# Performance work log

Measured on AMD Instinct MI355X. Metric: run time of the kernel, lower is better.

Reference implementation:

```python
import jax, jax.numpy as jnp
import numpy as np

B, S, D, H, N = 1024, 2, 1, 128, 128  # batch, static_size, dynamic_size, hidden, num_nodes


def setup_inputs() -> dict:
    key = jax.random.key(0)
    ks = jax.random.split(key, 16)

    def xav(k, shape):
        fan = shape[0] + shape[1]
        lim = jnp.sqrt(6.0 / fan)
        return jax.random.uniform(k, shape, jnp.float32, -lim, lim)

    return {
        "static": jax.random.uniform(ks[0], (B, S, N), jnp.float32),
        "dynamic": jax.random.uniform(ks[1], (B, D, N), jnp.float32),
        # encoders (Conv1d kernel_size=1 == pointwise linear)
        "enc_s_w": xav(ks[2], (H, S)), "enc_s_b": jnp.zeros((H,), jnp.float32),
        "enc_d_w": xav(ks[3], (H, D)), "enc_d_b": jnp.zeros((H,), jnp.float32),
        # decoder params
        "x0": xav(ks[4], (1, S)),
        "emb_w": xav(ks[5], (H, S)), "emb_b": jnp.zeros((H,), jnp.float32),
        "w_ih": xav(ks[6], (3 * H, H)), "w_hh": xav(ks[7], (3 * H, H)),
        "b_ih": jnp.zeros((3 * H,), jnp.float32), "b_hh": jnp.zeros((3 * H,), jnp.float32),
        "attn_v": xav(ks[8], (1, H)), "attn_W": xav(ks[9], (H, 3 * H)),
        "dec_v": xav(ks[10], (1, H)), "dec_W": xav(ks[11], (H, 2 * H)),
    }


def _gru_cell(x, h, w_ih, w_hh, b_ih, b_hh):
    gi = x @ w_ih.T + b_ih  # [B, 3H]
    gh = h @ w_hh.T + b_hh
    i_r, i_z, i_n = jnp.split(gi, 3, axis=-1)
    h_r, h_z, h_n = jnp.split(gh, 3, axis=-1)
    r = jax.nn.sigmoid(i_r + h_r)
    z = jax.nn.sigmoid(i_z + h_z)
    n = jnp.tanh(i_n + r * h_n)
    return (1.0 - z) * n + z * h


def reference(static, dynamic, enc_s_w, enc_s_b, enc_d_w, enc_d_b, x0,
              emb_w, emb_b, w_ih, w_hh, b_ih, b_hh, attn_v, attn_W, dec_v, dec_W):
    # encoders: pointwise conv
    static_enc = jnp.einsum('hs,bsn->bhn', enc_s_w, static) + enc_s_b[None, :, None]
    dynamic_enc = jnp.einsum('hd,bdn->bhn', enc_d_w, dynamic) + enc_d_b[None, :, None]

    h0 = jnp.zeros((static.shape[0], H), jnp.float32)
    out0 = jnp.broadcast_to(x0, (static.shape[0], S))

    def step(carry, _):
        h, last_out = carry
        emb = last_out @ emb_w.T + emb_b                     # [B,H]
        h = _gru_cell(emb, h, w_ih, w_hh, b_ih, b_hh)        # [B,H]
        hid = jnp.broadcast_to(h[:, :, None], static_enc.shape)
        energy = jnp.concatenate([static_enc, dynamic_enc, hid], axis=1)   # [B,3H,N]
        u = jnp.tanh(jnp.einsum('hk,bkn->bhn', attn_W, energy))
        attn = jax.nn.softmax(jnp.einsum('h,bhn->bn', attn_v[0], u), axis=1)
        context = jnp.einsum('bn,bhn->bh', attn, static_enc)
        ctx = jnp.broadcast_to(context[:, :, None], static_enc.shape)
        energy2 = jnp.concatenate([static_enc, ctx], axis=1)               # [B,2H,N]
        u2 = jnp.tanh(jnp.einsum('hk,bkn->bhn', dec_W, energy2))
        logits = jnp.einsum('h,bhn->bn', dec_v[0], u2)
        probs = jax.nn.softmax(logits, axis=1)  # mask is all-ones -> log(mask)=0
        ptr = jnp.argmax(probs, axis=1)                       # [B]
        logp = jnp.log(jnp.max(probs, axis=1))
        last_out = jnp.take_along_axis(static, ptr[:, None, None], axis=2)[:, :, 0]
        return (h, last_out), (ptr, logp)

    (_, _), (ptrs, logps) = jax.lax.scan(step, (h0, out0), None, length=N)
    tour_idx = ptrs.T            # [B, N]
    tour_logp = logps.T.sum(axis=1)  # [B]
    return tour_idx, tour_logp
```

## Files before the change

kernel.cpp:

```cpp
#include <hip/hip_runtime.h>


#define H128 128
#define N128 128
#define B1024 1024
#define SC 2.885390081777927f

__device__ __forceinline__ float sigmoid_acc(float x){
    return 1.f / (1.f + expf(-x));
}
__device__ __forceinline__ float tanh_ps(float xs){
    float e = exp2f(xs);
    float r = __builtin_amdgcn_rcpf(e + 1.f);
    return fmaf(-2.f, r, 1.f);
}

__global__ void prep_kernel(const float* __restrict__ enc_s_w, const float* __restrict__ enc_s_b,
                            const float* __restrict__ enc_d_w, const float* __restrict__ enc_d_b,
                            const float* __restrict__ emb_w,   const float* __restrict__ emb_b,
                            const float* __restrict__ w_ih,    const float* __restrict__ b_ih,
                            const float* __restrict__ b_hh,
                            const float* __restrict__ attn_v,  const float* __restrict__ attn_W,
                            const float* __restrict__ dec_v,   const float* __restrict__ dec_W,
                            float4* __restrict__ A4, float4* __restrict__ D4,
                            float4* __restrict__ Q4, float4* __restrict__ G4)
{
    const int tid = threadIdx.x;
    const int blk = blockIdx.x;
    if (blk < 3){
        const int j = blk*128 + tid;
        const float* w = w_ih + j*H128;
        float a = 0.f, b = 0.f, c = 0.f;
        for (int k = 0; k < H128; ++k){
            float wv = w[k];
            a = fmaf(wv, emb_w[2*k],   a);
            b = fmaf(wv, emb_w[2*k+1], b);
            c = fmaf(wv, emb_b[k],     c);
        }
        G4[j] = make_float4(a, b, c + b_ih[j], b_hh[j]);
    } else {
        const int h = tid;
        const float* aw = attn_W + h*384;
        float u0=0.f, u1=0.f, u2=0.f, c1=0.f;
        for (int k = 0; k < H128; ++k){
            float w = aw[k];
            u0 = fmaf(w, enc_s_w[2*k],   u0);
            u1 = fmaf(w, enc_s_w[2*k+1], u1);
            c1 = fmaf(w, enc_s_b[k],     c1);
        }
        for (int k = 0; k < H128; ++k){
            float w = aw[128+k];
            u2 = fmaf(w, enc_d_w[k], u2);
            c1 = fmaf(w, enc_d_b[k], c1);
        }
        A4[h] = make_float4(SC*u0, SC*u1, SC*u2, attn_v[h]);
        const float* dw = dec_W + h*256;
        float v0=0.f, v1=0.f, c2=0.f, q0=0.f, q1=0.f;
        for (int k = 0; k < H128; ++k){
            float w = dw[k];
            v0 = fmaf(w, enc_s_w[2*k],   v0);
            v1 = fmaf(w, enc_s_w[2*k+1], v1);
            c2 = fmaf(w, enc_s_b[k],     c2);
        }
        for (int k = 0; k < H128; ++k){
            float w = dw[128+k];
            q0 = fmaf(w, enc_s_w[2*k],   q0);
            q1 = fmaf(w, enc_s_w[2*k+1], q1);
            c2 = fmaf(w, enc_s_b[k],     c2);
        }
        D4[h] = make_float4(SC*v0, SC*v1, dec_v[h], 0.f);
        Q4[h] = make_float4(SC*q0, SC*q1, SC*c2, SC*c1);
    }
}

__global__ void tp_kernel(const float* __restrict__ whh, const float* __restrict__ attnW,
                          float* __restrict__ WT, float* __restrict__ AT)
{
    const int idx = blockIdx.x*256 + threadIdx.x;
    if (idx < 49152){
        const int k = idx / 384, r = idx - k*384;
        WT[idx] = whh[r*H128 + k];
    } else {
        const int i2 = idx - 49152;
        const int k = i2 >> 7, j = i2 & 127;
        AT[i2] = SC * attnW[j*384 + 256 + k];
    }
}

__global__ __launch_bounds__(256, 2)
void decode_kernel(const float* __restrict__ statc, const float* __restrict__ dyn,
                   const float* __restrict__ x0,
                   const float* __restrict__ WT, const float* __restrict__ AT,
                   const float4* __restrict__ A4g, const float4* __restrict__ D4g,
                   const float4* __restrict__ Q4g, const float4* __restrict__ G4g,
                   float* __restrict__ out)
{
    __shared__ __align__(16) float hbuf[2][2][H128];
    __shared__ float gpre[2][5][H128];
    __shared__ __align__(16) float ahl[2][H128], chl[2][H128];
    __shared__ float s0l[2][N128], s1l[2][N128];
    __shared__ float red[2][2][8];

    const int tid = threadIdx.x;
    const int g   = tid >> 7;
    const int jl  = tid & 127;
    const int wv  = (tid >> 6) & 1;
    const int b   = blockIdx.x*2 + g;

    const int  gate1 = tid >> 7;
    const int  j1    = tid & 127;
    const bool loA   = (tid < 128);
    const float4 Gv1 = G4g[tid];
    const float4 Gv2 = G4g[256 + j1];

    const float4 qv = Q4g[jl];
    const float q0r = qv.x, q1r = qv.y, c2r = qv.z, c1r = qv.w;

    const float s0n = statc[b*256 + jl];
    const float s1n = statc[b*256 + 128 + jl];
    const float d0n = dyn[b*128 + jl];
    s0l[g][jl] = s0n; s1l[g][jl] = s1n;
    hbuf[0][g][jl] = 0.f;
    float hreg = 0.f;
    float l00 = x0[0], l01 = x0[1];
    float l10 = l00,   l11 = l01;

    float logp = 0.f;
    int cur = 0;
    __syncthreads();

    for (int t = 0; t < N128; ++t){
        const float4* h0v = (const float4*)&hbuf[cur][0][0];
        const float4* h1v = (const float4*)&hbuf[cur][1][0];
        {
            const float* pW = WT + tid;
            float a0 = 0.f, a1 = 0.f;
            #pragma unroll 4
            for (int k4 = 0; k4 < 32; ++k4){
                float4 h0 = h0v[k4], h1 = h1v[k4];
                float w0 = pW[(4*k4+0)*384];
                float w1 = pW[(4*k4+1)*384];
                float w2 = pW[(4*k4+2)*384];
                float w3 = pW[(4*k4+3)*384];
                a0 = fmaf(w0,h0.x, fmaf(w1,h0.y, fmaf(w2,h0.z, fmaf(w3,h0.w, a0))));
                a1 = fmaf(w0,h1.x, fmaf(w1,h1.y, fmaf(w2,h1.z, fmaf(w3,h1.w, a1))));
            }
            float gi0 = fmaf(Gv1.x, l00, fmaf(Gv1.y, l01, Gv1.z));
            float gi1 = fmaf(Gv1.x, l10, fmaf(Gv1.y, l11, Gv1.z));
            gpre[0][gate1][j1] = gi0 + (a0 + Gv1.w);
            gpre[1][gate1][j1] = gi1 + (a1 + Gv1.w);
        }
        {
            const float* pW = WT + 256 + j1;
            const int koff = gate1 * 16;
            float a0 = 0.f, a1 = 0.f;
            #pragma unroll 4
            for (int ki = 0; ki < 16; ++ki){
                const int k4 = koff + ki;
                float4 h0 = h0v[k4], h1 = h1v[k4];
                float w0 = pW[(4*k4+0)*384];
                float w1 = pW[(4*k4+1)*384];
                float w2 = pW[(4*k4+2)*384];
                float w3 = pW[(4*k4+3)*384];
                a0 = fmaf(w0,h0.x, fmaf(w1,h0.y, fmaf(w2,h0.z, fmaf(w3,h0.w, a0))));
                a1 = fmaf(w0,h1.x, fmaf(w1,h1.y, fmaf(w2,h1.z, fmaf(w3,h1.w, a1))));
            }
            if (loA){
                gpre[0][2][j1] = a0 + Gv2.w;
                gpre[1][2][j1] = a1 + Gv2.w;
                gpre[0][3][j1] = fmaf(Gv2.x, l00, fmaf(Gv2.y, l01, Gv2.z));
                gpre[1][3][j1] = fmaf(Gv2.x, l10, fmaf(Gv2.y, l11, Gv2.z));
            } else {
                gpre[0][4][j1] = a0;
                gpre[1][4][j1] = a1;
            }
        }
        __syncthreads();
        {
            float r  = sigmoid_acc(gpre[g][0][jl]);
            float z  = sigmoid_acc(gpre[g][1][jl]);
            float accn = gpre[g][2][jl] + gpre[g][4][jl];
            float nn = tanhf(gpre[g][3][jl] + r * accn);
            float hnew = (1.f - z) * nn + z * hreg;
            hbuf[cur^1][g][jl] = hnew; hreg = hnew;
        }
        __syncthreads();
        cur ^= 1;
        {
            const float4* hn4 = (const float4*)&hbuf[cur][g][0];
            const float* pA = AT + jl;
            float acc = c1r;
            #pragma unroll 4
            for (int k4 = 0; k4 < 32; ++k4){
                float4 hv = hn4[k4];
                acc = fmaf(pA[(4*k4+0)*128], hv.x, acc);
                acc = fmaf(pA[(4*k4+1)*128], hv.y, acc);
                acc = fmaf(pA[(4*k4+2)*128], hv.z, acc);
                acc = fmaf(pA[(4*k4+3)*128], hv.w, acc);
            }
            ahl[g][jl] = acc;
        }
        __syncthreads();
        const float4* ah4 = (const float4*)&ahl[g][0];
        float sc = 0.f;
        #pragma unroll 2
        for (int k = 0; k < 32; ++k){
            float4 ah = ah4[k];
            { float4 a = A4g[4*k+0]; float tt = fmaf(a.x,s0n, fmaf(a.y,s1n, fmaf(a.z,d0n, ah.x))); sc = fmaf(tanh_ps(tt), a.w, sc); }
            { float4 a = A4g[4*k+1]; float tt = fmaf(a.x,s0n, fmaf(a.y,s1n, fmaf(a.z,d0n, ah.y))); sc = fmaf(tanh_ps(tt), a.w, sc); }
            { float4 a = A4g[4*k+2]; float tt = fmaf(a.x,s0n, fmaf(a.y,s1n, fmaf(a.z,d0n, ah.z))); sc = fmaf(tanh_ps(tt), a.w, sc); }
            { float4 a = A4g[4*k+3]; float tt = fmaf(a.x,s0n, fmaf(a.y,s1n, fmaf(a.z,d0n, ah.w))); sc = fmaf(tanh_ps(tt), a.w, sc); }
        }
        float e  = __expf(sc);
        float se = e, sa = e * s0n, sb = e * s1n;
        #pragma unroll
        for (int off = 32; off > 0; off >>= 1){
            se += __shfl_xor(se, off, 64);
            sa += __shfl_xor(sa, off, 64);
            sb += __shfl_xor(sb, off, 64);
        }
        if ((tid & 63) == 0){ red[g][wv][0]=se; red[g][wv][1]=sa; red[g][wv][2]=sb; }
        __syncthreads();
        {
            float ssum = red[g][0][0] + red[g][1][0];
            float sat  = red[g][0][1] + red[g][1][1];
            float sbt  = red[g][0][2] + red[g][1][2];
            float cs0 = sat / ssum;
            float cs1 = sbt / ssum;
            chl[g][jl] = fmaf(q0r, cs0, fmaf(q1r, cs1, c2r));
        }
        __syncthreads();
        const float4* ch4 = (const float4*)&chl[g][0];
        float lg = 0.f;
        #pragma unroll 2
        for (int k = 0; k < 32; ++k){
            float4 ch = ch4[k];
            { float4 dd = D4g[4*k+0]; float tt = fmaf(dd.x,s0n, fmaf(dd.y,s1n, ch.x)); lg = fmaf(tanh_ps(tt), dd.z, lg); }
            { float4 dd = D4g[4*k+1]; float tt = fmaf(dd.x,s0n, fmaf(dd.y,s1n, ch.y)); lg = fmaf(tanh_ps(tt), dd.z, lg); }
            { float4 dd = D4g[4*k+2]; float tt = fmaf(dd.x,s0n, fmaf(dd.y,s1n, ch.z)); lg = fmaf(tanh_ps(tt), dd.z, lg); }
            { float4 dd = D4g[4*k+3]; float tt = fmaf(dd.x,s0n, fmaf(dd.y,s1n, ch.w)); lg = fmaf(tanh_ps(tt), dd.z, lg); }
        }
        float v = lg; int bi = jl;
        #pragma unroll
        for (int off = 32; off > 0; off >>= 1){
            float ov = __shfl_xor(v, off, 64);
            int   oi = __shfl_xor(bi, off, 64);
            if (ov > v || (ov == v && oi < bi)){ v = ov; bi = oi; }
        }
        float e2 = __expf(lg - v);
        #pragma unroll
        for (int off = 32; off > 0; off >>= 1) e2 += __shfl_xor(e2, off, 64);
        if ((tid & 63) == 0){ red[g][wv][4]=v; red[g][wv][5]=__int_as_float(bi); red[g][wv][6]=e2; }
        __syncthreads();
        int ptrs[2];
        #pragma unroll
        for (int gg = 0; gg < 2; ++gg){
            float va = red[gg][0][4], vb = red[gg][1][4];
            int   ia = __float_as_int(red[gg][0][5]), ib = __float_as_int(red[gg][1][5]);
            ptrs[gg] = (va > vb || (va == vb && ia < ib)) ? ia : ib;
        }
        {
            float va = red[g][0][4], vb = red[g][1][4];
            int   ia = __float_as_int(red[g][0][5]), ib = __float_as_int(red[g][1][5]);
            float s2a = red[g][0][6], s2b = red[g][1][6];
            float m2; int ptr;
            if (va > vb || (va == vb && ia < ib)){ m2 = va; ptr = ia; } else { m2 = vb; ptr = ib; }
            float sum2 = fmaf(s2a, __expf(va - m2), s2b * __expf(vb - m2));
            logp -= logf(sum2);
            if (jl == 0) out[b*N128 + t] = (float)ptr;
        }
        l00 = s0l[0][ptrs[0]]; l01 = s1l[0][ptrs[0]];
        l10 = s0l[1][ptrs[1]]; l11 = s1l[1][ptrs[1]];
    }
    if (jl == 0) out[B1024*N128 + b] = logp;
}

extern "C" void kernel_launch(void* const* d_in, const int* in_sizes, int n_in,
                              void* d_out, int out_size, void* d_ws, size_t ws_size,
                              hipStream_t stream)
{
    const float* statc   = (const float*)d_in[0];
    const float* dyn     = (const float*)d_in[1];
    const float* enc_s_w = (const float*)d_in[2];
    const float* enc_s_b = (const float*)d_in[3];
    const float* enc_d_w = (const float*)d_in[4];
    const float* enc_d_b = (const float*)d_in[5];
    const float* x0      = (const float*)d_in[6];
    const float* emb_w   = (const float*)d_in[7];
    const float* emb_b   = (const float*)d_in[8];
    const float* w_ih    = (const float*)d_in[9];
    const float* w_hh    = (const float*)d_in[10];
    const float* b_ih    = (const float*)d_in[11];
    const float* b_hh    = (const float*)d_in[12];
    const float* attn_v  = (const float*)d_in[13];
    const float* attn_W  = (const float*)d_in[14];
    const float* dec_v   = (const float*)d_in[15];
    const float* dec_W   = (const float*)d_in[16];

    float* ws = (float*)d_ws;
    float4* A4 = (float4*)(ws);
    float4* D4 = (float4*)(ws + 512);
    float4* Q4 = (float4*)(ws + 1024);
    float4* G4 = (float4*)(ws + 1536);
    float*  WT = ws + 3072;
    float*  AT = ws + 3072 + 49152;

    prep_kernel<<<dim3(4), dim3(128), 0, stream>>>(
        enc_s_w, enc_s_b, enc_d_w, enc_d_b, emb_w, emb_b,
        w_ih, b_ih, b_hh, attn_v, attn_W, dec_v, dec_W,
        A4, D4, Q4, G4);

    tp_kernel<<<dim3(256), dim3(256), 0, stream>>>(w_hh, attn_W, WT, AT);

    decode_kernel<<<dim3(B1024/2), dim3(256), 0, stream>>>(
        statc, dyn, x0, WT, AT,
        A4, D4, Q4, G4, (float*)d_out);
}
```

Baseline: 2.755 ms.

## Double threads per block by splitting reductions over k across thread halves

The decode kernel now runs 512 threads per block instead of 256. Each GRU matvec, attention projection and the two tanh-score loops have their k-range split across two or four thread groups, with partial sums written to shared memory and combined by the first 256 threads. The aim is to shorten the serial per-step critical path of the 128-step recurrence by adding parallelism. In exchange it adds extra __syncthreads barriers and shared-memory partial-sum traffic, leaves half the threads idle during the elementwise and reduction phases, and tightens the register budget through the new launch bounds.

```diff
diff --git a/kernel.cpp b/kernel.cpp
--- a/kernel.cpp
+++ b/kernel.cpp
@@ -87,7 +87,7 @@
     }
 }
 
-__global__ __launch_bounds__(256, 2)
+__global__ __launch_bounds__(512, 4)
 void decode_kernel(const float* __restrict__ statc, const float* __restrict__ dyn,
                    const float* __restrict__ x0,
                    const float* __restrict__ WT, const float* __restrict__ AT,
@@ -96,36 +96,43 @@
                    float* __restrict__ out)
 {
     __shared__ __align__(16) float hbuf[2][2][H128];
-    __shared__ float gpre[2][5][H128];
-    __shared__ __align__(16) float ahl[2][H128], chl[2][H128];
+    __shared__ float gprz[2][2][256];
+    __shared__ float gprn[2][4][H128];
+    __shared__ float ahp[2][4][H128];
+    __shared__ __align__(16) float ahl[2][H128];
+    __shared__ __align__(16) float chl[2][H128];
+    __shared__ float scp[2][2][H128];
     __shared__ float s0l[2][N128], s1l[2][N128];
     __shared__ float red[2][2][8];
 
     const int tid = threadIdx.x;
-    const int g   = tid >> 7;
-    const int jl  = tid & 127;
-    const int wv  = (tid >> 6) & 1;
-    const int b   = blockIdx.x*2 + g;
-
-    const int  gate1 = tid >> 7;
-    const int  j1    = tid & 127;
-    const bool loA   = (tid < 128);
-    const float4 Gv1 = G4g[tid];
-    const float4 Gv2 = G4g[256 + j1];
-
-    const float4 qv = Q4g[jl];
-    const float q0r = qv.x, q1r = qv.y, c2r = qv.z, c1r = qv.w;
-
-    const float s0n = statc[b*256 + jl];
-    const float s1n = statc[b*256 + 128 + jl];
-    const float d0n = dyn[b*128 + jl];
-    s0l[g][jl] = s0n; s1l[g][jl] = s1n;
-    hbuf[0][g][jl] = 0.f;
-    float hreg = 0.f;
-    float l00 = x0[0], l01 = x0[1];
-    float l10 = l00,   l11 = l01;
-
-    float logp = 0.f;
+    const int mg  = tid >> 8;
+    const int mn  = tid & 127;
+    const int hi  = (tid >> 7) & 1;
+    const int q   = (tid >> 7) & 3;
+    const int rowa  = tid & 255;
+    const int halfa = mg;
+    const int b0  = blockIdx.x*2;
+
+    const float s0n = statc[(b0+mg)*256 + mn];
+    const float s1n = statc[(b0+mg)*256 + 128 + mn];
+    const float d0n = dyn[(b0+mg)*128 + mn];
+    s0l[mg][mn] = s0n; s1l[mg][mn] = s1n;
+
+    const int cg = tid >> 7;
+    const int cn = tid & 127;
+    const int wvi = (tid >> 6) & 1;
+    float4 Gr = make_float4(0,0,0,0), Gz = Gr, Gn = Gr, qv = Gr;
+    float cs0n = 0.f, cs1n = 0.f, hreg = 0.f, lA = 0.f, lB = 0.f, logp = 0.f;
+    if (tid < 256){
+        Gr = G4g[cn]; Gz = G4g[128+cn]; Gn = G4g[256+cn];
+        qv = Q4g[cn];
+        cs0n = statc[(b0+cg)*256 + cn];
+        cs1n = statc[(b0+cg)*256 + 128 + cn];
+        hbuf[0][cg][cn] = 0.f;
+        lA = x0[0]; lB = x0[1];
+    }
+
     int cur = 0;
     __syncthreads();
 
@@ -133,10 +140,11 @@
         const float4* h0v = (const float4*)&hbuf[cur][0][0];
         const float4* h1v = (const float4*)&hbuf[cur][1][0];
         {
-            const float* pW = WT + tid;
+            const float* pW = WT + rowa;
             float a0 = 0.f, a1 = 0.f;
             #pragma unroll 4
-            for (int k4 = 0; k4 < 32; ++k4){
+            for (int ki = 0; ki < 16; ++ki){
+                const int k4 = halfa*16 + ki;
                 float4 h0 = h0v[k4], h1 = h1v[k4];
                 float w0 = pW[(4*k4+0)*384];
                 float w1 = pW[(4*k4+1)*384];
@@ -145,18 +153,15 @@
                 a0 = fmaf(w0,h0.x, fmaf(w1,h0.y, fmaf(w2,h0.z, fmaf(w3,h0.w, a0))));
                 a1 = fmaf(w0,h1.x, fmaf(w1,h1.y, fmaf(w2,h1.z, fmaf(w3,h1.w, a1))));
             }
-            float gi0 = fmaf(Gv1.x, l00, fmaf(Gv1.y, l01, Gv1.z));
-            float gi1 = fmaf(Gv1.x, l10, fmaf(Gv1.y, l11, Gv1.z));
-            gpre[0][gate1][j1] = gi0 + (a0 + Gv1.w);
-            gpre[1][gate1][j1] = gi1 + (a1 + Gv1.w);
-        }
-        {
-            const float* pW = WT + 256 + j1;
-            const int koff = gate1 * 16;
+            gprz[0][halfa][rowa] = a0;
+            gprz[1][halfa][rowa] = a1;
+        }
+        {
+            const float* pW = WT + 256 + mn;
             float a0 = 0.f, a1 = 0.f;
             #pragma unroll 4
-            for (int ki = 0; ki < 16; ++ki){
-                const int k4 = koff + ki;
+            for (int ki = 0; ki < 8; ++ki){
+                const int k4 = q*8 + ki;
                 float4 h0 = h0v[k4], h1 = h1v[k4];
                 float w0 = pW[(4*k4+0)*384];
                 float w1 = pW[(4*k4+1)*384];
@@ -165,114 +170,130 @@
                 a0 = fmaf(w0,h0.x, fmaf(w1,h0.y, fmaf(w2,h0.z, fmaf(w3,h0.w, a0))));
                 a1 = fmaf(w0,h1.x, fmaf(w1,h1.y, fmaf(w2,h1.z, fmaf(w3,h1.w, a1))));
             }
-            if (loA){
-                gpre[0][2][j1] = a0 + Gv2.w;
-                gpre[1][2][j1] = a1 + Gv2.w;
-                gpre[0][3][j1] = fmaf(Gv2.x, l00, fmaf(Gv2.y, l01, Gv2.z));
-                gpre[1][3][j1] = fmaf(Gv2.x, l10, fmaf(Gv2.y, l11, Gv2.z));
-            } else {
-                gpre[0][4][j1] = a0;
-                gpre[1][4][j1] = a1;
-            }
-        }
-        __syncthreads();
-        {
-            float r  = sigmoid_acc(gpre[g][0][jl]);
-            float z  = sigmoid_acc(gpre[g][1][jl]);
-            float accn = gpre[g][2][jl] + gpre[g][4][jl];
-            float nn = tanhf(gpre[g][3][jl] + r * accn);
+            gprn[0][q][mn] = a0;
+            gprn[1][q][mn] = a1;
+        }
+        __syncthreads();
+        if (tid < 256){
+            float accr = gprz[cg][0][cn]     + gprz[cg][1][cn];
+            float accz = gprz[cg][0][128+cn] + gprz[cg][1][128+cn];
+            float accn = (gprn[cg][0][cn]+gprn[cg][1][cn]) + (gprn[cg][2][cn]+gprn[cg][3][cn]);
+            float gir = fmaf(Gr.x, lA, fmaf(Gr.y, lB, Gr.z));
+            float giz = fmaf(Gz.x, lA, fmaf(Gz.y, lB, Gz.z));
+            float gin = fmaf(Gn.x, lA, fmaf(Gn.y, lB, Gn.z));
+            float r  = sigmoid_acc(gir + (accr + Gr.w));
+            float z  = sigmoid_acc(giz + (accz + Gz.w));
+            float nn = tanhf(gin + r * (accn + Gn.w));
             float hnew = (1.f - z) * nn + z * hreg;
-            hbuf[cur^1][g][jl] = hnew; hreg = hnew;
+            hbuf[cur^1][cg][cn] = hnew; hreg = hnew;
         }
         __syncthreads();
         cur ^= 1;
         {
-            const float4* hn4 = (const float4*)&hbuf[cur][g][0];
-            const float* pA = AT + jl;
-            float acc = c1r;
+            const float4* hn0 = (const float4*)&hbuf[cur][0][0];
+            const float4* hn1 = (const float4*)&hbuf[cur][1][0];
+            const float* pA = AT + mn;
+            float a0 = 0.f, a1 = 0.f;
             #pragma unroll 4
-            for (int k4 = 0; k4 < 32; ++k4){
-                float4 hv = hn4[k4];
-                acc = fmaf(pA[(4*k4+0)*128], hv.x, acc);
-                acc = fmaf(pA[(4*k4+1)*128], hv.y, acc);
-                acc = fmaf(pA[(4*k4+2)*128], hv.z, acc);
-                acc = fmaf(pA[(4*k4+3)*128], hv.w, acc);
-            }
-            ahl[g][jl] = acc;
-        }
-        __syncthreads();
-        const float4* ah4 = (const float4*)&ahl[g][0];
-        float sc = 0.f;
-        #pragma unroll 2
-        for (int k = 0; k < 32; ++k){
-            float4 ah = ah4[k];
-            { float4 a = A4g[4*k+0]; float tt = fmaf(a.x,s0n, fmaf(a.y,s1n, fmaf(a.z,d0n, ah.x))); sc = fmaf(tanh_ps(tt), a.w, sc); }
-            { float4 a = A4g[4*k+1]; float tt = fmaf(a.x,s0n, fmaf(a.y,s1n, fmaf(a.z,d0n, ah.y))); sc = fmaf(tanh_ps(tt), a.w, sc); }
-            { float4 a = A4g[4*k+2]; float tt = fmaf(a.x,s0n, fmaf(a.y,s1n, fmaf(a.z,d0n, ah.z))); sc = fmaf(tanh_ps(tt), a.w, sc); }
-            { float4 a = A4g[4*k+3]; float tt = fmaf(a.x,s0n, fmaf(a.y,s1n, fmaf(a.z,d0n, ah.w))); sc = fmaf(tanh_ps(tt), a.w, sc); }
-        }
-        float e  = __expf(sc);
-        float se = e, sa = e * s0n, sb = e * s1n;
-        #pragma unroll
-        for (int off = 32; off > 0; off >>= 1){
-            se += __shfl_xor(se, off, 64);
-            sa += __shfl_xor(sa, off, 64);
-            sb += __shfl_xor(sb, off, 64);
-        }
-        if ((tid & 63) == 0){ red[g][wv][0]=se; red[g][wv][1]=sa; red[g][wv][2]=sb; }
-        __syncthreads();
-        {
-            float ssum = red[g][0][0] + red[g][1][0];
-            float sat  = red[g][0][1] + red[g][1][1];
-            float sbt  = red[g][0][2] + red[g][1][2];
+            for (int ki = 0; ki < 8; ++ki){
+                const int k4 = q*8 + ki;
+                float4 hv0 = hn0[k4], hv1 = hn1[k4];
+                float w0 = pA[(4*k4+0)*128];
+                float w1 = pA[(4*k4+1)*128];
+                float w2 = pA[(4*k4+2)*128];
+                float w3 = pA[(4*k4+3)*128];
+                a0 = fmaf(w0,hv0.x, fmaf(w1,hv0.y, fmaf(w2,hv0.z, fmaf(w3,hv0.w, a0))));
+                a1 = fmaf(w0,hv1.x, fmaf(w1,hv1.y, fmaf(w2,hv1.z, fmaf(w3,hv1.w, a1))));
+            }
+            ahp[0][q][mn] = a0;
+            ahp[1][q][mn] = a1;
+        }
+        __syncthreads();
+        if (tid < 256){
+            ahl[cg][cn] = ((ahp[cg][0][cn]+ahp[cg][1][cn]) + (ahp[cg][2][cn]+ahp[cg][3][cn])) + qv.w;
+        }
+        __syncthreads();
+        {
+            const float4* ah4 = (const float4*)&ahl[mg][0];
+            float sc = 0.f;
+            #pragma unroll 2
+            for (int kk = 0; kk < 16; ++kk){
+                const int k = hi*16 + kk;
+                float4 ah = ah4[k];
+                { float4 a = A4g[4*k+0]; float tt = fmaf(a.x,s0n, fmaf(a.y,s1n, fmaf(a.z,d0n, ah.x))); sc = fmaf(tanh_ps(tt), a.w, sc); }
+                { float4 a = A4g[4*k+1]; float tt = fmaf(a.x,s0n, fmaf(a.y,s1n, fmaf(a.z,d0n, ah.y))); sc = fmaf(tanh_ps(tt), a.w, sc); }
+                { float4 a = A4g[4*k+2]; float tt = fmaf(a.x,s0n, fmaf(a.y,s1n, fmaf(a.z,d0n, ah.z))); sc = fmaf(tanh_ps(tt), a.w, sc); }
+                { float4 a = A4g[4*k+3]; float tt = fmaf(a.x,s0n, fmaf(a.y,s1n, fmaf(a.z,d0n, ah.w))); sc = fmaf(tanh_ps(tt), a.w, sc); }
+            }
+            scp[mg][hi][mn] = sc;
+        }
+        __syncthreads();
+        if (tid < 256){
+            float sc = scp[cg][0][cn] + scp[cg][1][cn];
+            float e  = __expf(sc);
+            float se = e, sa = e * cs0n, sb = e * cs1n;
+            #pragma unroll
+            for (int off = 32; off > 0; off >>= 1){
+                se += __shfl_xor(se, off, 64);
+                sa += __shfl_xor(sa, off, 64);
+                sb += __shfl_xor(sb, off, 64);
+            }
+            if ((tid & 63) == 0){ red[cg][wvi][0]=se; red[cg][wvi][1]=sa; red[cg][wvi][2]=sb; }
+        }
+        __syncthreads();
+        if (tid < 256){
+            float ssum = red[cg][0][0] + red[cg][1][0];
+            float sat  = red[cg][0][1] + red[cg][1][1];
+            float sbt  = red[cg][0][2] + red[cg][1][2];
             float cs0 = sat / ssum;
             float cs1 = sbt / ssum;
-            chl[g][jl] = fmaf(q0r, cs0, fmaf(q1r, cs1, c2r));
-        }
-        __syncthreads();
-        const float4* ch4 = (const float4*)&chl[g][0];
-        float lg = 0.f;
-        #pragma unroll 2
-        for (int k = 0; k < 32; ++k){
-            float4 ch = ch4[k];
-            { float4 dd = D4g[4*k+0]; float tt = fmaf(dd.x,s0n, fmaf(dd.y,s1n, ch.x)); lg = fmaf(tanh_ps(tt), dd.z, lg); }
-            { float4 dd = D4g[4*k+1]; float tt = fmaf(dd.x,s0n, fmaf(dd.y,s1n, ch.y)); lg = fmaf(tanh_ps(tt), dd.z, lg); }
-            { float4 dd = D4g[4*k+2]; float tt = fmaf(dd.x,s0n, fmaf(dd.y,s1n, ch.z)); lg = fmaf(tanh_ps(tt), dd.z, lg); }
-            { float4 dd = D4g[4*k+3]; float tt = fmaf(dd.x,s0n, fmaf(dd.y,s1n, ch.w)); lg = fmaf(tanh_ps(tt), dd.z, lg); }
-        }
-        float v = lg; int bi = jl;
-        #pragma unroll
-        for (int off = 32; off > 0; off >>= 1){
-            float ov = __shfl_xor(v, off, 64);
-            int   oi = __shfl_xor(bi, off, 64);
-            if (ov > v || (ov == v && oi < bi)){ v = ov; bi = oi; }
-        }
-        float e2 = __expf(lg - v);
-        #pragma unroll
-        for (int off = 32; off > 0; off >>= 1) e2 += __shfl_xor(e2, off, 64);
-        if ((tid & 63) == 0){ red[g][wv][4]=v; red[g][wv][5]=__int_as_float(bi); red[g][wv][6]=e2; }
-        __syncthreads();
-        int ptrs[2];
-        #pragma unroll
-        for (int gg = 0; gg < 2; ++gg){
-            float va = red[gg][0][4], vb = red[gg][1][4];
-            int   ia = __float_as_int(red[gg][0][5]), ib = __float_as_int(red[gg][1][5]);
-            ptrs[gg] = (va > vb || (va == vb && ia < ib)) ? ia : ib;
-        }
-        {
-            float va = red[g][0][4], vb = red[g][1][4];
-            int   ia = __float_as_int(red[g][0][5]), ib = __float_as_int(red[g][1][5]);
-            float s2a = red[g][0][6], s2b = red[g][1][6];
+            chl[cg][cn] = fmaf(qv.x, cs0, fmaf(qv.y, cs1, qv.z));
+        }
+        __syncthreads();
+        {
+            const float4* ch4 = (const float4*)&chl[mg][0];
+            float lg = 0.f;
+            #pragma unroll 2
+            for (int kk = 0; kk < 16; ++kk){
+                const int k = hi*16 + kk;
+                float4 ch = ch4[k];
+                { float4 dd = D4g[4*k+0]; float tt = fmaf(dd.x,s0n, fmaf(dd.y,s1n, ch.x)); lg = fmaf(tanh_ps(tt), dd.z, lg); }
+                { float4 dd = D4g[4*k+1]; float tt = fmaf(dd.x,s0n, fmaf(dd.y,s1n, ch.y)); lg = fmaf(tanh_ps(tt), dd.z, lg); }
+                { float4 dd = D4g[4*k+2]; float tt = fmaf(dd.x,s0n, fmaf(dd.y,s1n, ch.z)); lg = fmaf(tanh_ps(tt), dd.z, lg); }
+                { float4 dd = D4g[4*k+3]; float tt = fmaf(dd.x,s0n, fmaf(dd.y,s1n, ch.w)); lg = fmaf(tanh_ps(tt), dd.z, lg); }
+            }
+            scp[mg][hi][mn] = lg;
+        }
+        __syncthreads();
+        if (tid < 256){
+            float lg = scp[cg][0][cn] + scp[cg][1][cn];
+            float v = lg; int bi = cn;
+            #pragma unroll
+            for (int off = 32; off > 0; off >>= 1){
+                float ov = __shfl_xor(v, off, 64);
+                int   oi = __shfl_xor(bi, off, 64);
+                if (ov > v || (ov == v && oi < bi)){ v = ov; bi = oi; }
+            }
+            float e2 = __expf(lg - v);
+            #pragma unroll
+            for (int off = 32; off > 0; off >>= 1) e2 += __shfl_xor(e2, off, 64);
+            if ((tid & 63) == 0){ red[cg][wvi][4]=v; red[cg][wvi][5]=__int_as_float(bi); red[cg][wvi][6]=e2; }
+        }
+        __syncthreads();
+        if (tid < 256){
+            float va = red[cg][0][4], vb = red[cg][1][4];
+            int   ia = __float_as_int(red[cg][0][5]), ib = __float_as_int(red[cg][1][5]);
+            float s2a = red[cg][0][6], s2b = red[cg][1][6];
             float m2; int ptr;
             if (va > vb || (va == vb && ia < ib)){ m2 = va; ptr = ia; } else { m2 = vb; ptr = ib; }
             float sum2 = fmaf(s2a, __expf(va - m2), s2b * __expf(vb - m2));
             logp -= logf(sum2);
-            if (jl == 0) out[b*N128 + t] = (float)ptr;
-        }
-        l00 = s0l[0][ptrs[0]]; l01 = s1l[0][ptrs[0]];
-        l10 = s0l[1][ptrs[1]]; l11 = s1l[1][ptrs[1]];
+            if (cn == 0) out[(b0+cg)*N128 + t] = (float)ptr;
+            lA = s0l[cg][ptr];
+            lB = s1l[cg][ptr];
+        }
     }
-    if (jl == 0) out[B1024*N128 + b] = logp;
+    if (tid < 256 && cn == 0) out[B1024*N128 + (b0+cg)] = logp;
 }
 
 extern "C" void kernel_launch(void* const* d_in, const int* in_sizes, int n_in,
@@ -312,7 +333,7 @@
 
     tp_kernel<<<dim3(256), dim3(256), 0, stream>>>(w_hh, attn_W, WT, AT);
 
-    decode_kernel<<<dim3(B1024/2), dim3(256), 0, stream>>>(
+    decode_kernel<<<dim3(B1024/2), dim3(512), 0, stream>>>(
         statc, dyn, x0, WT, AT,
         A4, D4, Q4, G4, (float*)d_out);
 }
```

Result: no change. 2.735 ms (-0.7%).
